# Kernel optimization log

Measured on AMD Instinct MI355X. Metric: run time of the kernel, lower is better.

Reference implementation:

```python
import jax, jax.numpy as jnp
import numpy as np

B, L, D = 8, 2048, 256
D_MODEL = 1024
NUM_SIGNALS = 16
MAX_POSITIONS = 4096
ROLE_OUTPUT = 2  # role id used for the CLS token


def setup_inputs() -> dict:
    key = jax.random.key(0)
    ks = jax.random.split(key, 12)
    emb = jax.random.normal(ks[0], (B, L, D), dtype=jnp.float32)
    pos = jax.random.randint(ks[1], (B, L), 1, MAX_POSITIONS + 1)          # pos >= 1 for real tokens
    sid = jax.random.randint(ks[2], (B, L), 0, NUM_SIGNALS)
    role = jax.random.randint(ks[3], (B, L), 0, 3)
    padding_mask = jax.random.uniform(ks[4], (B, L)) < 0.75                # True = real token
    # learned parameters
    proj_W = jax.random.normal(ks[5], (NUM_SIGNALS, D_MODEL, D), dtype=jnp.float32) * (1.0 / np.sqrt(D))
    proj_b = jax.random.normal(ks[6], (NUM_SIGNALS, D_MODEL), dtype=jnp.float32) * 0.01
    cls_content = jax.random.normal(ks[7], (D_MODEL,), dtype=jnp.float32)
    pos_embed = jax.random.normal(ks[8], (MAX_POSITIONS + 1, D_MODEL), dtype=jnp.float32)
    id_embed = jax.random.normal(ks[9], (NUM_SIGNALS + 1, D_MODEL), dtype=jnp.float32)
    role_embed = jax.random.normal(ks[10], (3, D_MODEL), dtype=jnp.float32)
    return dict(emb=emb, pos=pos, sid=sid, role=role, padding_mask=padding_mask,
                proj_W=proj_W, proj_b=proj_b, cls_content=cls_content,
                pos_embed=pos_embed, id_embed=id_embed, role_embed=role_embed)


def reference(emb, pos, sid, role, padding_mask,
              proj_W, proj_b, cls_content, pos_embed, id_embed, role_embed):
    Bv, Lv, _ = emb.shape
    S, d_model, _ = proj_W.shape
    cls_id = S

    # Grouped per-signal projection: one GEMM per signal id, select per token.
    tokens = jnp.zeros((Bv, Lv, d_model), dtype=emb.dtype)
    for s in range(S):
        proj_s = jnp.einsum('bld,ed->ble', emb, proj_W[s]) + proj_b[s]   # (B, L, d_model)
        keep = ((sid == s) & padding_mask)[..., None]
        tokens = jnp.where(keep, proj_s, tokens)

    # Prepend CLS
    cls = jnp.broadcast_to(cls_content[None, None, :], (Bv, 1, d_model))
    tokens = jnp.concatenate([cls, tokens], axis=1)                       # (B, L+1, d_model)

    pos_full = jnp.concatenate([jnp.zeros((Bv, 1), dtype=pos.dtype), pos], axis=1)
    sid_full = jnp.concatenate([jnp.full((Bv, 1), cls_id, dtype=sid.dtype), sid], axis=1)
    role_full = jnp.concatenate([jnp.full((Bv, 1), ROLE_OUTPUT, dtype=role.dtype), role], axis=1)

    tokens = tokens + pos_embed[pos_full] + id_embed[sid_full] + role_embed[role_full]

    attn_keep = jnp.concatenate([jnp.ones((Bv, 1), dtype=bool), padding_mask], axis=1)
    return tokens, attn_keep
```

## Files before the change

### kernel.cpp

```cpp
#include <hip/hip_runtime.h>
#include <hip/hip_bf16.h>
#include <stdint.h>

#define B_ 8
#define L_ 2048
#define NTOK 16384
#define DK 256
#define DM 1024
#define NS 16
#define LOUT 2049
#define TOK_OUT (B_*LOUT*DM)
#define ATTN_OUT (B_*LOUT)
#define PCAP 2048
#define UCAP 8192

typedef unsigned short u16;
typedef unsigned int u32;
typedef __bf16 bf16x8 __attribute__((ext_vector_type(8)));
typedef float f32x4 __attribute__((ext_vector_type(4)));

__device__ inline u32 packbf2(float lo, float hi) {
    u32 a, b;
    __builtin_memcpy(&a, &lo, 4);
    __builtin_memcpy(&b, &hi, 4);
    a = (a + 0x8000u) >> 16;
    b = (b + 0x8000u) & 0xFFFF0000u;
    return a | b;
}

__device__ inline void gll16(const void* g, void* l) {
    __builtin_amdgcn_global_load_lds(
        (const __attribute__((address_space(1))) unsigned int*)g,
        (__attribute__((address_space(3))) unsigned int*)l, 16, 0, 0);
}

#define WS_CUR 0
#define WS_UCUR 16
#define WS_WIDTH 32
#define WS_PERM 64
#define WS_UNM (64 + NS * PCAP)
#define EMB_OFF 262144ULL
#define W_OFF (EMB_OFF + 16384ULL * 512ULL)
#define WS_NEED (W_OFF + 16384ULL * 512ULL)

__device__ inline int sniff_width(const unsigned char* mb, int tid, int* sh) {
    if (tid == 0) { sh[0] = 0; sh[1] = 0; sh[2] = 0; }
    __syncthreads();
    int c1ge2 = 0, ge2 = 0, oddnz = 0;
    const u32* mw = (const u32*)mb;
    #pragma unroll
    for (int i = 0; i < 16; i++) {
        u32 x = mw[tid * 16 + i];
        u32 b0 = x & 0xFF, b1 = (x >> 8) & 0xFF, b2 = (x >> 16) & 0xFF, b3 = x >> 24;
        if (b1 >= 2) c1ge2 = 1;
        if (b0 >= 2 || b1 >= 2 || b2 >= 2 || b3 >= 2) ge2 = 1;
        if ((b1 | b3) != 0) oddnz = 1;
    }
    if (c1ge2) atomicOr(&sh[0], 1);
    if (ge2) atomicOr(&sh[1], 1);
    if (oddnz) atomicOr(&sh[2], 1);
    __syncthreads();
    if (sh[0]) return 2;
    if (sh[1]) return 4;
    if (sh[2]) return 1;
    return 4;
}

__device__ inline int decode_mask(const unsigned char* mb, int t, int width) {
    if (width == 1) return mb[t] != 0;
    if (width == 2) return ((const u16*)mb)[t] != 0;
    return ((const u32*)mb)[t] != 0;
}

#define SORT_B 64
#define PREP_GRID (SORT_B + 1024)

__global__ __launch_bounds__(256) void prep_all(
    const unsigned char* __restrict__ mb, const int* __restrict__ sid,
    const float* __restrict__ emb, const float* __restrict__ W,
    int* __restrict__ wsi, unsigned char* __restrict__ wsb) {
    __shared__ int sh[3];
    __shared__ int lcnt[NS], gbase[NS];
    __shared__ int lcnt_u, gbase_u;
    int bid = blockIdx.x;
    int tid = threadIdx.x;
    int lane = tid & 63;
    int wv = tid >> 6;

    if (bid < SORT_B) {
        if (tid < NS) lcnt[tid] = 0;
        if (tid == 0) lcnt_u = 0;
        int width = sniff_width(mb, tid, sh);
        if (bid == 0 && tid == 0) wsi[WS_WIDTH] = width;
        int t = bid * 256 + tid;
        int m = decode_mask(mb, t, width);
        int s = sid[t];
        int lr;
        if (m) lr = atomicAdd(&lcnt[s], 1);
        else   lr = atomicAdd(&lcnt_u, 1);
        __syncthreads();
        if (tid < NS) gbase[tid] = atomicAdd(&wsi[WS_CUR + tid], lcnt[tid]);
        if (tid == 0) gbase_u = atomicAdd(&wsi[WS_UCUR], lcnt_u);
        __syncthreads();
        if (m) {
            int r = gbase[s] + lr;
            if (r < PCAP) wsi[WS_PERM + s * PCAP + r] = t;
        } else {
            int r = gbase_u + lr;
            if (r < UCAP) wsi[WS_UNM + r] = t;
        }
        return;
    }

    int cb = bid - SORT_B;
    const float* src;
    u16* dst;
    if (cb < 512) {
        src = emb;
        dst = (u16*)(wsb + EMB_OFF);
    } else {
        cb -= 512;
        src = W;
        dst = (u16*)(wsb + W_OFF);
    }
    int r0 = cb * 32 + wv * 8;
    #pragma unroll 4
    for (int i = 0; i < 8; i++) {
        int r = r0 + i;
        float4 a = *(const float4*)(src + (size_t)r * DK + lane * 4);
        uint2 o;
        o.x = packbf2(a.x, a.y);
        o.y = packbf2(a.z, a.w);
        *(uint2*)(dst + (size_t)r * DK + lane * 4) = o;
    }
}

#define GG 1280
#define CLS_B0 (GG - 67)
#define ATTN_B0 (GG - 65)
#define EPAD 132

__global__ __launch_bounds__(256, 4) void gemm_big(
    const unsigned char* __restrict__ mb,
    const int* __restrict__ pos, const int* __restrict__ sid,
    const int* __restrict__ role,
    const float* __restrict__ bias, const float* __restrict__ cls,
    const float* __restrict__ pos_emb, const float* __restrict__ id_emb,
    const float* __restrict__ role_emb,
    const int* __restrict__ wsi, const unsigned char* __restrict__ wsb,
    float* __restrict__ out) {
    __shared__ unsigned char smem[64 * EPAD * 4];
    __shared__ int toks[128];
    u16 (*As)[128 * 32] = (u16(*)[128 * 32])smem;
    u16 (*Bs)[128 * 32] = (u16(*)[128 * 32])(smem + 16384);
    float* etile = (float*)smem;
    int bi = (int)blockIdx.x;
    int tid = threadIdx.x;
    int lane = tid & 63;
    int wv = tid >> 6;

    int cnts[NS];
    int mtot = 0;
    #pragma unroll
    for (int i = 0; i < NS; i++) {
        int c = wsi[WS_CUR + i];
        cnts[i] = c > PCAP ? PCAP : c;
        mtot += (cnts[i] + 127) >> 7;
    }
    int xcd = bi & 7;
    int j = bi >> 3;
    int m_lo = (xcd * mtot) >> 3;
    int m_hi = ((xcd + 1) * mtot) >> 3;
    int cm = m_hi - m_lo;
    bool doGemm = (cm > 0 && j < cm * 8);
    int s = -1, lrt = 0, n0 = 0;
    if (doGemm) {
        int nt = j / cm;
        int m = m_lo + (j - nt * cm);
        n0 = nt << 7;
        #pragma unroll
        for (int i = 0; i < NS; i++) {
            int rt = (cnts[i] + 127) >> 7;
            if (s < 0) {
                if (m < rt) { s = i; lrt = m; }
                else m -= rt;
            }
        }
        if (s < 0) doGemm = false;
    }

    if (doGemm) {
        int rowsValid = cnts[s] - lrt * 128;
        if (rowsValid > 128) rowsValid = 128;

        if (tid < 128) {
            int base = WS_PERM + s * PCAP + lrt * 128;
            toks[tid] = wsi[base + ((tid < rowsValid) ? tid : 0)];
        }
        __syncthreads();

        const u16* Eb = (const u16*)(wsb + EMB_OFF);
        const u16* Bb = (const u16*)(wsb + W_OFF) + (size_t)(s * DM + n0) * DK;

        int srow = lane >> 2;
        int slseg = lane & 3;
        int arow = wv * 16 + srow;
        int ags = (slseg - (arow >> 1)) & 3;
        const u16* AsrcLo = Eb + (size_t)toks[arow] * DK;
        const u16* AsrcHi = Eb + (size_t)toks[arow + 64] * DK;

        f32x4 acc[4][4];
        #pragma unroll
        for (int im = 0; im < 4; im++)
            #pragma unroll
            for (int jn = 0; jn < 4; jn++) acc[im][jn] = (f32x4){0.f, 0.f, 0.f, 0.f};

        int wm = wv & 1, wn = wv >> 1;
        int mcol = lane & 15;
        int quad = lane >> 4;

#define STAGE(kc, bf)                                                          \
        {                                                                      \
            gll16(AsrcLo + (kc) * 32 + ags * 8, &As[bf][(wv * 16) * 32]);      \
            gll16(AsrcHi + (kc) * 32 + ags * 8, &As[bf][(64 + wv * 16) * 32]); \
            gll16(Bb + (size_t)arow * DK + (kc) * 32 + ags * 8,                \
                  &Bs[bf][(wv * 16) * 32]);                                    \
            gll16(Bb + (size_t)(64 + arow) * DK + (kc) * 32 + ags * 8,         \
                  &Bs[bf][(64 + wv * 16) * 32]);                               \
        }

        STAGE(0, 0)
        #pragma unroll
        for (int kc = 0; kc < 8; ++kc) {
            __syncthreads();
            if (kc < 7) STAGE(kc + 1, (kc + 1) & 1)
            int bf = kc & 1;
            bf16x8 af[4], bfr[4];
            #pragma unroll
            for (int im = 0; im < 4; im++) {
                int row = wm * 64 + im * 16 + mcol;
                int sg = (quad + (row >> 1)) & 3;
                af[im] = *(const bf16x8*)(&As[bf][row * 32 + sg * 8]);
            }
            #pragma unroll
            for (int jn = 0; jn < 4; jn++) {
                int row = wn * 64 + jn * 16 + mcol;
                int sg = (quad + (row >> 1)) & 3;
                bfr[jn] = *(const bf16x8*)(&Bs[bf][row * 32 + sg * 8]);
            }
            #pragma unroll
            for (int im = 0; im < 4; im++)
                #pragma unroll
                for (int jn = 0; jn < 4; jn++)
                    acc[im][jn] = __builtin_amdgcn_mfma_f32_16x16x32_bf16(
                        af[im], bfr[jn], acc[im][jn], 0, 0, 0);
        }
#undef STAGE

        int ecol = (lane & 31) * 4;
        int rp = lane >> 5;
        f32x4 bc4 = *(const f32x4*)(bias + (size_t)s * DM + n0 + ecol);
        f32x4 ic4 = *(const f32x4*)(id_emb + (size_t)s * DM + n0 + ecol);
        f32x4 bi4 = bc4 + ic4;

        __syncthreads();
        #pragma unroll
        for (int h = 0; h < 2; h++) {
            #pragma unroll
            for (int imh = 0; imh < 2; imh++) {
                int im = h * 2 + imh;
                #pragma unroll
                for (int jn = 0; jn < 4; jn++) {
                    int col = wn * 64 + jn * 16 + mcol;
                    #pragma unroll
                    for (int r = 0; r < 4; r++) {
                        int er = imh * 32 + wm * 16 + quad * 4 + r;
                        etile[er * EPAD + col] = acc[im][jn][r];
                    }
                }
            }
            __syncthreads();
            #pragma unroll
            for (int p = 0; p < 8; p++) {
                int er = wv * 16 + p * 2 + rp;
                int rowT = ((er >> 4) & 1) * 64 + (h * 2 + (er >> 5)) * 16
                           + (er & 15);
                if (rowT < rowsValid) {
                    int t = toks[rowT];
                    int pz = pos[t];
                    int ro = role[t];
                    int b = t >> 11, l = t & 2047;
                    size_t orow = (size_t)(b * LOUT + l + 1) * DM + n0 + ecol;
                    f32x4 av = *(const f32x4*)&etile[er * EPAD + ecol];
                    f32x4 pv = *(const f32x4*)(pos_emb + (size_t)pz * DM + n0 + ecol);
                    f32x4 rv = *(const f32x4*)(role_emb + (size_t)ro * DM + n0 + ecol);
                    f32x4 o = av + bi4 + pv + rv;
                    __builtin_nontemporal_store(o, (f32x4*)(out + orow));
                }
            }
            __syncthreads();
        }
    }

    {
        int ucnt = wsi[WS_UCUR];
        if (ucnt > UCAP) ucnt = UCAP;
        for (int idx = (GG - 1 - bi) * 4 + wv; idx < ucnt; idx += GG * 4) {
            int t = wsi[WS_UNM + idx];
            int p = pos[t], sd = sid[t], ro = role[t];
            int b = t >> 11, l = t & 2047;
            size_t orow = (size_t)(b * LOUT + l + 1) * DM;
            const float* pr = pos_emb + (size_t)p * DM;
            const float* ir = id_emb + (size_t)sd * DM;
            const float* rr = role_emb + (size_t)ro * DM;
            #pragma unroll
            for (int it = 0; it < 4; it++) {
                int c = it * 256 + lane * 4;
                f32x4 a = *(const f32x4*)(pr + c);
                f32x4 d = *(const f32x4*)(ir + c);
                f32x4 e = *(const f32x4*)(rr + c);
                f32x4 o = a + d + e;
                __builtin_nontemporal_store(o, (f32x4*)(out + orow + c));
            }
        }
        if (bi >= CLS_B0 && bi < ATTN_B0) {
            int b = (bi - CLS_B0) * 4 + wv;
            size_t orow = (size_t)(b * LOUT) * DM;
            #pragma unroll
            for (int it = 0; it < 4; it++) {
                int c = it * 256 + lane * 4;
                f32x4 cc = *(const f32x4*)(cls + c);
                f32x4 a = *(const f32x4*)(pos_emb + c);
                f32x4 d = *(const f32x4*)(id_emb + NS * DM + c);
                f32x4 e = *(const f32x4*)(role_emb + 2 * DM + c);
                f32x4 o = cc + a + d + e;
                *(f32x4*)(out + orow + c) = o;
            }
        }
        if (bi >= ATTN_B0) {
            int width = wsi[WS_WIDTH];
            int i = (bi - ATTN_B0) * 256 + tid;
            if (i < ATTN_OUT) {
                int b = i / LOUT;
                int jj = i - b * LOUT;
                float val = (jj == 0) ? 1.0f
                    : (float)decode_mask(mb, b * L_ + jj - 1, width);
                out[TOK_OUT + i] = val;
            }
        }
    }
}

extern "C" void kernel_launch(void* const* d_in, const int* in_sizes, int n_in,
                              void* d_out, int out_size, void* d_ws, size_t ws_size,
                              hipStream_t stream) {
    const float* emb = (const float*)d_in[0];
    const int* pos = (const int*)d_in[1];
    const int* sid = (const int*)d_in[2];
    const int* role = (const int*)d_in[3];
    const unsigned char* mask = (const unsigned char*)d_in[4];
    const float* W = (const float*)d_in[5];
    const float* bias = (const float*)d_in[6];
    const float* cls = (const float*)d_in[7];
    const float* pos_emb = (const float*)d_in[8];
    const float* id_emb = (const float*)d_in[9];
    const float* role_emb = (const float*)d_in[10];
    float* out = (float*)d_out;
    int* wsi = (int*)d_ws;
    unsigned char* wsb = (unsigned char*)d_ws;

    (void)hipMemsetAsync(wsi, 0, 64 * sizeof(int), stream);
    hipLaunchKernelGGL(prep_all, dim3(PREP_GRID), dim3(256), 0, stream,
                       mask, sid, emb, W, wsi, wsb);
    hipLaunchKernelGGL(gemm_big, dim3(GG), dim3(256), 0, stream,
                       mask, pos, sid, role, bias, cls, pos_emb, id_emb,
                       role_emb, wsi, wsb, out);
}
```

Before: 155.0 us.

## Shrink GEMM tiles to 64x64 with one-row-strip-per-warp layout and higher occupancy

The grouped GEMM tile drops from 128x128 to 64x64 and the grid grows to match. Each warp now owns a 16-row strip across all 64 columns. Launch bounds rise to 8 blocks per CU and shared memory per block shrinks. Because each warp writes and reads only its own rows of the epilogue staging tile, the epilogue drops the block-wide barriers between those steps. The aim is more blocks in flight to hide the latency of the gather-heavy, memory-bound epilogue, at the cost of less operand reuse per tile and more redundant loads of weights and embeddings.

```diff
diff --git a/kernel.cpp b/kernel.cpp
--- a/kernel.cpp
+++ b/kernel.cpp
@@ -135,12 +135,12 @@
     }
 }
 
-#define GG 1280
+#define GG 4608
 #define CLS_B0 (GG - 67)
 #define ATTN_B0 (GG - 65)
-#define EPAD 132
-
-__global__ __launch_bounds__(256, 4) void gemm_big(
+#define EPAD 68
+
+__global__ __launch_bounds__(256, 8) void gemm_big(
     const unsigned char* __restrict__ mb,
     const int* __restrict__ pos, const int* __restrict__ sid,
     const int* __restrict__ role,
@@ -150,9 +150,9 @@
     const int* __restrict__ wsi, const unsigned char* __restrict__ wsb,
     float* __restrict__ out) {
     __shared__ unsigned char smem[64 * EPAD * 4];
-    __shared__ int toks[128];
-    u16 (*As)[128 * 32] = (u16(*)[128 * 32])smem;
-    u16 (*Bs)[128 * 32] = (u16(*)[128 * 32])(smem + 16384);
+    __shared__ int toks[64];
+    u16 (*As)[64 * 32] = (u16(*)[64 * 32])smem;
+    u16 (*Bs)[64 * 32] = (u16(*)[64 * 32])(smem + 8192);
     float* etile = (float*)smem;
     int bi = (int)blockIdx.x;
     int tid = threadIdx.x;
@@ -165,22 +165,22 @@
     for (int i = 0; i < NS; i++) {
         int c = wsi[WS_CUR + i];
         cnts[i] = c > PCAP ? PCAP : c;
-        mtot += (cnts[i] + 127) >> 7;
+        mtot += (cnts[i] + 63) >> 6;
     }
     int xcd = bi & 7;
     int j = bi >> 3;
     int m_lo = (xcd * mtot) >> 3;
     int m_hi = ((xcd + 1) * mtot) >> 3;
     int cm = m_hi - m_lo;
-    bool doGemm = (cm > 0 && j < cm * 8);
+    bool doGemm = (cm > 0 && j < cm * 16);
     int s = -1, lrt = 0, n0 = 0;
     if (doGemm) {
         int nt = j / cm;
         int m = m_lo + (j - nt * cm);
-        n0 = nt << 7;
+        n0 = nt << 6;
         #pragma unroll
         for (int i = 0; i < NS; i++) {
-            int rt = (cnts[i] + 127) >> 7;
+            int rt = (cnts[i] + 63) >> 6;
             if (s < 0) {
                 if (m < rt) { s = i; lrt = m; }
                 else m -= rt;
@@ -190,11 +190,11 @@
     }
 
     if (doGemm) {
-        int rowsValid = cnts[s] - lrt * 128;
-        if (rowsValid > 128) rowsValid = 128;
-
-        if (tid < 128) {
-            int base = WS_PERM + s * PCAP + lrt * 128;
+        int rowsValid = cnts[s] - lrt * 64;
+        if (rowsValid > 64) rowsValid = 64;
+
+        if (tid < 64) {
+            int base = WS_PERM + s * PCAP + lrt * 64;
             toks[tid] = wsi[base + ((tid < rowsValid) ? tid : 0)];
         }
         __syncthreads();
@@ -206,27 +206,20 @@
         int slseg = lane & 3;
         int arow = wv * 16 + srow;
         int ags = (slseg - (arow >> 1)) & 3;
-        const u16* AsrcLo = Eb + (size_t)toks[arow] * DK;
-        const u16* AsrcHi = Eb + (size_t)toks[arow + 64] * DK;
-
-        f32x4 acc[4][4];
-        #pragma unroll
-        for (int im = 0; im < 4; im++)
-            #pragma unroll
-            for (int jn = 0; jn < 4; jn++) acc[im][jn] = (f32x4){0.f, 0.f, 0.f, 0.f};
-
-        int wm = wv & 1, wn = wv >> 1;
+        const u16* Asrc = Eb + (size_t)toks[arow] * DK;
+
+        f32x4 acc[4];
+        #pragma unroll
+        for (int jn = 0; jn < 4; jn++) acc[jn] = (f32x4){0.f, 0.f, 0.f, 0.f};
+
         int mcol = lane & 15;
         int quad = lane >> 4;
 
 #define STAGE(kc, bf)                                                          \
         {                                                                      \
-            gll16(AsrcLo + (kc) * 32 + ags * 8, &As[bf][(wv * 16) * 32]);      \
-            gll16(AsrcHi + (kc) * 32 + ags * 8, &As[bf][(64 + wv * 16) * 32]); \
+            gll16(Asrc + (kc) * 32 + ags * 8, &As[bf][(wv * 16) * 32]);        \
             gll16(Bb + (size_t)arow * DK + (kc) * 32 + ags * 8,                \
                   &Bs[bf][(wv * 16) * 32]);                                    \
-            gll16(Bb + (size_t)(64 + arow) * DK + (kc) * 32 + ags * 8,         \
-                  &Bs[bf][(64 + wv * 16) * 32]);                               \
         }
 
         STAGE(0, 0)
@@ -235,70 +228,55 @@
             __syncthreads();
             if (kc < 7) STAGE(kc + 1, (kc + 1) & 1)
             int bf = kc & 1;
-            bf16x8 af[4], bfr[4];
-            #pragma unroll
-            for (int im = 0; im < 4; im++) {
-                int row = wm * 64 + im * 16 + mcol;
+            bf16x8 af, bfr[4];
+            {
+                int row = wv * 16 + mcol;
                 int sg = (quad + (row >> 1)) & 3;
-                af[im] = *(const bf16x8*)(&As[bf][row * 32 + sg * 8]);
+                af = *(const bf16x8*)(&As[bf][row * 32 + sg * 8]);
             }
             #pragma unroll
             for (int jn = 0; jn < 4; jn++) {
-                int row = wn * 64 + jn * 16 + mcol;
+                int row = jn * 16 + mcol;
                 int sg = (quad + (row >> 1)) & 3;
                 bfr[jn] = *(const bf16x8*)(&Bs[bf][row * 32 + sg * 8]);
             }
             #pragma unroll
-            for (int im = 0; im < 4; im++)
-                #pragma unroll
-                for (int jn = 0; jn < 4; jn++)
-                    acc[im][jn] = __builtin_amdgcn_mfma_f32_16x16x32_bf16(
-                        af[im], bfr[jn], acc[im][jn], 0, 0, 0);
+            for (int jn = 0; jn < 4; jn++)
+                acc[jn] = __builtin_amdgcn_mfma_f32_16x16x32_bf16(
+                    af, bfr[jn], acc[jn], 0, 0, 0);
         }
 #undef STAGE
 
-        int ecol = (lane & 31) * 4;
-        int rp = lane >> 5;
+        int ecol = (lane & 15) * 4;
+        int rp = lane >> 4;
         f32x4 bc4 = *(const f32x4*)(bias + (size_t)s * DM + n0 + ecol);
         f32x4 ic4 = *(const f32x4*)(id_emb + (size_t)s * DM + n0 + ecol);
         f32x4 bi4 = bc4 + ic4;
 
         __syncthreads();
         #pragma unroll
-        for (int h = 0; h < 2; h++) {
-            #pragma unroll
-            for (int imh = 0; imh < 2; imh++) {
-                int im = h * 2 + imh;
-                #pragma unroll
-                for (int jn = 0; jn < 4; jn++) {
-                    int col = wn * 64 + jn * 16 + mcol;
-                    #pragma unroll
-                    for (int r = 0; r < 4; r++) {
-                        int er = imh * 32 + wm * 16 + quad * 4 + r;
-                        etile[er * EPAD + col] = acc[im][jn][r];
-                    }
-                }
-            }
-            __syncthreads();
-            #pragma unroll
-            for (int p = 0; p < 8; p++) {
-                int er = wv * 16 + p * 2 + rp;
-                int rowT = ((er >> 4) & 1) * 64 + (h * 2 + (er >> 5)) * 16
-                           + (er & 15);
-                if (rowT < rowsValid) {
-                    int t = toks[rowT];
-                    int pz = pos[t];
-                    int ro = role[t];
-                    int b = t >> 11, l = t & 2047;
-                    size_t orow = (size_t)(b * LOUT + l + 1) * DM + n0 + ecol;
-                    f32x4 av = *(const f32x4*)&etile[er * EPAD + ecol];
-                    f32x4 pv = *(const f32x4*)(pos_emb + (size_t)pz * DM + n0 + ecol);
-                    f32x4 rv = *(const f32x4*)(role_emb + (size_t)ro * DM + n0 + ecol);
-                    f32x4 o = av + bi4 + pv + rv;
-                    __builtin_nontemporal_store(o, (f32x4*)(out + orow));
-                }
-            }
-            __syncthreads();
+        for (int jn = 0; jn < 4; jn++) {
+            #pragma unroll
+            for (int r = 0; r < 4; r++) {
+                int er = wv * 16 + quad * 4 + r;
+                etile[er * EPAD + jn * 16 + mcol] = acc[jn][r];
+            }
+        }
+        #pragma unroll
+        for (int p = 0; p < 4; p++) {
+            int er = wv * 16 + p * 4 + rp;
+            if (er < rowsValid) {
+                int t = toks[er];
+                int pz = pos[t];
+                int ro = role[t];
+                int b = t >> 11, l = t & 2047;
+                size_t orow = (size_t)(b * LOUT + l + 1) * DM + n0 + ecol;
+                f32x4 av = *(const f32x4*)&etile[er * EPAD + ecol];
+                f32x4 pv = *(const f32x4*)(pos_emb + (size_t)pz * DM + n0 + ecol);
+                f32x4 rv = *(const f32x4*)(role_emb + (size_t)ro * DM + n0 + ecol);
+                f32x4 o = av + bi4 + pv + rv;
+                __builtin_nontemporal_store(o, (f32x4*)(out + orow));
+            }
         }
     }
 
```

New measurement: 155.4 us. No clear change (+0.3%).
